# Kernel optimization log

Measured on AMD Instinct MI355X. Metric: run time of the kernel, lower is better.

The kernel has to match this reference:

```python
import jax, jax.numpy as jnp
import numpy as np
from functools import partial

EPS = 1e-8

@partial(jax.custom_vjp, nondiff_argnums=(2, 3))
def ste_quantize(x, scale, clamp_min, clamp_max):
    # forward: clamp(round(x/scale), min, max); backward: grad/scale (STE)
    return jnp.clip(jnp.round(x / scale), clamp_min, clamp_max)

def _ste_fwd(x, scale, clamp_min, clamp_max):
    return ste_quantize(x, scale, clamp_min, clamp_max), scale

def _ste_bwd(clamp_min, clamp_max, scale, g):
    return (g / scale, jnp.zeros_like(scale))

ste_quantize.defvjp(_ste_fwd, _ste_bwd)


def setup_inputs() -> dict:
    key = jax.random.key(0)
    kx, kw = jax.random.split(key)
    x = jax.random.normal(kx, (4, 4096, 2048), dtype=jnp.float32)
    # nn.init.normal_(weight, mean=0.0, std=0.006)
    weight = 0.006 * jax.random.normal(kw, (2048, 2048), dtype=jnp.float32)
    return {"x": x, "weight": weight}


def reference(x, weight):
    # per-tensor ternary weight quantization: alpha = mean(|W|)
    alpha = jnp.maximum(jnp.mean(jnp.abs(weight)), EPS)
    w_q = ste_quantize(weight, alpha, -1.0, 1.0)  # (out, in), values in {-1,0,1}
    # per-token int8 activation quantization: beta = max(|x|)/127
    beta = jnp.maximum(jnp.max(jnp.abs(x), axis=-1, keepdims=True) / 127.0, EPS)  # (b,s,1)
    x_q = ste_quantize(x, beta, -127.0, 127.0)  # (b,s,in)
    # fp32 GEMM on quantized values, then dequant rescale
    y = jnp.einsum('bsi,oi->bso', x_q, w_q)
    return y * alpha * beta
```

## Files before the change

kernel.cpp:

```cpp
#include <hip/hip_runtime.h>

#define IN_DIM 2048
#define OUT_DIM 2048
#define EPS 1e-8f

#define BK 128
#define NKT (IN_DIM / BK)
#define HALF 16384

using int32x4 = __attribute__((ext_vector_type(4))) int;

__global__ __launch_bounds__(256) void absum_kernel(const float* __restrict__ w,
                                                    double* __restrict__ sum, int n4) {
    int tid = blockIdx.x * blockDim.x + threadIdx.x;
    int stride = gridDim.x * blockDim.x;
    float s = 0.f;
    for (int i = tid; i < n4; i += stride) {
        float4 v = ((const float4*)w)[i];
        s += fabsf(v.x) + fabsf(v.y) + fabsf(v.z) + fabsf(v.w);
    }
    for (int off = 32; off; off >>= 1) s += __shfl_down(s, off);
    __shared__ float wsum[4];
    int lane = threadIdx.x & 63, wave = threadIdx.x >> 6;
    if (lane == 0) wsum[wave] = s;
    __syncthreads();
    if (threadIdx.x == 0) {
        double t = (double)wsum[0] + (double)wsum[1] + (double)wsum[2] + (double)wsum[3];
        atomicAdd(sum, t);
    }
}

__global__ __launch_bounds__(256) void quantw_kernel(const float* __restrict__ w,
                                                     const double* __restrict__ sumptr,
                                                     signed char* __restrict__ wq,
                                                     float* __restrict__ alpha_out, int n4) {
    float alpha = fmaxf((float)(*sumptr * (1.0 / (double)(IN_DIM * OUT_DIM))), EPS);
    int i = blockIdx.x * blockDim.x + threadIdx.x;
    if (i == 0) *alpha_out = alpha;
    if (i >= n4) return;
    float4 v = ((const float4*)w)[i];
    char4 q;
    q.x = (signed char)fminf(fmaxf(rintf(v.x / alpha), -1.f), 1.f);
    q.y = (signed char)fminf(fmaxf(rintf(v.y / alpha), -1.f), 1.f);
    q.z = (signed char)fminf(fmaxf(rintf(v.z / alpha), -1.f), 1.f);
    q.w = (signed char)fminf(fmaxf(rintf(v.w / alpha), -1.f), 1.f);
    ((char4*)wq)[i] = q;
}

__global__ __launch_bounds__(256) void quantx_kernel(const float* __restrict__ x,
                                                     signed char* __restrict__ xq,
                                                     float* __restrict__ beta_arr,
                                                     int tokens) {
    const int lane = threadIdx.x & 63;
    const int wave = threadIdx.x >> 6;
    const int t = blockIdx.x * 4 + wave;
    if (t >= tokens) return;

    const float4* row = (const float4*)(x + (size_t)t * IN_DIM);
    float4 v[8];
    float m = 0.f;
#pragma unroll
    for (int j = 0; j < 8; ++j) {
        v[j] = row[lane + 64 * j];
        m = fmaxf(m, fmaxf(fmaxf(fabsf(v[j].x), fabsf(v[j].y)),
                           fmaxf(fabsf(v[j].z), fabsf(v[j].w))));
    }
#pragma unroll
    for (int off = 32; off; off >>= 1) m = fmaxf(m, __shfl_xor(m, off));
    const float beta = fmaxf(m * (1.f / 127.f), EPS);
    if (lane == 0) beta_arr[t] = beta;

    char4* orow = (char4*)(xq + (size_t)t * IN_DIM);
#pragma unroll
    for (int j = 0; j < 8; ++j) {
        char4 q;
        q.x = (signed char)fminf(fmaxf(rintf(v[j].x / beta), -127.f), 127.f);
        q.y = (signed char)fminf(fmaxf(rintf(v[j].y / beta), -127.f), 127.f);
        q.z = (signed char)fminf(fmaxf(rintf(v[j].z / beta), -127.f), 127.f);
        q.w = (signed char)fminf(fmaxf(rintf(v[j].w / beta), -127.f), 127.f);
        orow[lane + 64 * j] = q;
    }
}

__device__ __forceinline__ void gll(const signed char* g, signed char* l) {
    __builtin_amdgcn_global_load_lds((const __attribute__((address_space(1))) void*)g,
        (__attribute__((address_space(3))) void*)l, 16, 0, 0);
}

#define CLUSTER(BASE, AF)                                                                      \
    __builtin_amdgcn_s_setprio(1);                                                             \
    _Pragma("unroll")                                                                          \
    for (int m_ = 0; m_ < 4; ++m_)                                                             \
        _Pragma("unroll")                                                                      \
        for (int n_ = 0; n_ < 4; ++n_)                                                         \
            acc[(BASE) + m_][n_] = __builtin_amdgcn_mfma_i32_16x16x64_i8(                      \
                AF[m_], bf[n_], acc[(BASE) + m_][n_], 0, 0, 0);                                \
    __builtin_amdgcn_s_setprio(0);

template<bool STG, bool TAIL>
__device__ __forceinline__ void ktile(int T, signed char* lds, int32x4 (&acc)[8][4],
                                      int aoff, int boff, int f0, int f1,
                                      const signed char* a0, const signed char* a1,
                                      const signed char* b0, const signed char* b1) {
    const int s = (T & 1) * HALF;
    const int d = ((T + 1) & 1) * HALF;
    const size_t ko = (size_t)(T + 1) * BK;
    int32x4 af0[4], af1[4], bf[4];

#pragma unroll
    for (int m = 0; m < 4; ++m) af0[m] = *(const int32x4*)(lds + s + aoff + m * 1024);
#pragma unroll
    for (int n = 0; n < 4; ++n) bf[n] = *(const int32x4*)(lds + 65536 + s + boff + n * 1024);
    if constexpr (STG) { gll(a0 + ko, lds + d + f0); gll(a1 + ko, lds + d + f1); }
#pragma unroll
    for (int m = 0; m < 4; ++m) af1[m] = *(const int32x4*)(lds + s + aoff + 4096 + m * 1024);
    CLUSTER(0, af0)
    if constexpr (STG) { gll(b0 + ko, lds + 65536 + d + f0); gll(b1 + ko, lds + 65536 + d + f1); }
    CLUSTER(4, af1)
    if constexpr (TAIL) asm volatile("s_waitcnt vmcnt(0)" ::: "memory");
    else                asm volatile("s_waitcnt vmcnt(4)" ::: "memory");
    __builtin_amdgcn_s_barrier();

#pragma unroll
    for (int m = 0; m < 4; ++m) af0[m] = *(const int32x4*)(lds + 32768 + s + aoff + m * 1024);
#pragma unroll
    for (int n = 0; n < 4; ++n) bf[n] = *(const int32x4*)(lds + 98304 + s + boff + n * 1024);
    if constexpr (STG) { gll(a0 + ko + 64, lds + 32768 + d + f0); gll(a1 + ko + 64, lds + 32768 + d + f1); }
#pragma unroll
    for (int m = 0; m < 4; ++m) af1[m] = *(const int32x4*)(lds + 32768 + s + aoff + 4096 + m * 1024);
    CLUSTER(0, af0)
    if constexpr (STG) { gll(b0 + ko + 64, lds + 98304 + d + f0); gll(b1 + ko + 64, lds + 98304 + d + f1); }
    CLUSTER(4, af1)
    if constexpr (!TAIL) {
        asm volatile("s_waitcnt vmcnt(4)" ::: "memory");
        __builtin_amdgcn_s_barrier();
    }
}

__global__ __launch_bounds__(512, 2) void gemm_kernel(const signed char* __restrict__ xq,
                                                      const signed char* __restrict__ wq,
                                                      const float* __restrict__ beta,
                                                      const float* __restrict__ alpha_p,
                                                      float* __restrict__ out) {
    extern __shared__ signed char lds[];
    const int tid = threadIdx.x;
    const int lane = tid & 63;
    const int wave = tid >> 6;
    const int wm = wave >> 2;
    const int wn = wave & 3;
    const int row0 = blockIdx.x * 256;
    const int col0 = blockIdx.y * 256;

    const int f0 = tid * 16;
    const int f1 = f0 + 8192;
    const int g0 = f0 >> 10, kg0 = (f0 >> 8) & 3, r0 = (f0 >> 4) & 15;
    const int g1 = f1 >> 10, kg1 = (f1 >> 8) & 3, r1 = (f1 >> 4) & 15;
    const signed char* a0 = xq + (size_t)(row0 + g0 * 16 + r0) * IN_DIM + kg0 * 16;
    const signed char* a1 = xq + (size_t)(row0 + g1 * 16 + r1) * IN_DIM + kg1 * 16;
    const signed char* b0 = wq + (size_t)(col0 + g0 * 16 + r0) * IN_DIM + kg0 * 16;
    const signed char* b1 = wq + (size_t)(col0 + g1 * 16 + r1) * IN_DIM + kg1 * 16;

    const int kr = (lane >> 4) * 256 + (lane & 15) * 16;
    const int aoff = wm * 8192 + kr;
    const int boff = wn * 4096 + kr;

    int32x4 acc[8][4] = {};

    gll(a0, lds + f0);              gll(a1, lds + f1);
    gll(b0, lds + 65536 + f0);      gll(b1, lds + 65536 + f1);
    gll(a0 + 64, lds + 32768 + f0); gll(a1 + 64, lds + 32768 + f1);
    gll(b0 + 64, lds + 98304 + f0); gll(b1 + 64, lds + 98304 + f1);
    asm volatile("s_waitcnt vmcnt(4)" ::: "memory");
    __builtin_amdgcn_s_barrier();

    for (int T = 0; T < NKT - 1; ++T)
        ktile<true, false>(T, lds, acc, aoff, boff, f0, f1, a0, a1, b0, b1);
    ktile<false, true>(NKT - 1, lds, acc, aoff, boff, f0, f1, a0, a1, b0, b1);

    const float alpha = *alpha_p;
#pragma unroll
    for (int mi = 0; mi < 8; ++mi) {
        int rbase = row0 + wm * 128 + mi * 16 + ((lane >> 4) << 2);
#pragma unroll
        for (int r = 0; r < 4; ++r) {
            int row = rbase + r;
            float scale = alpha * beta[row];
#pragma unroll
            for (int n = 0; n < 4; ++n) {
                int col = col0 + wn * 64 + n * 16 + (lane & 15);
                out[(size_t)row * OUT_DIM + col] = (float)acc[mi][n][r] * scale;
            }
        }
    }
}

extern "C" void kernel_launch(void* const* d_in, const int* in_sizes, int n_in,
                              void* d_out, int out_size, void* d_ws, size_t ws_size,
                              hipStream_t stream) {
    const float* x = (const float*)d_in[0];
    const float* w = (const float*)d_in[1];
    float* out = (float*)d_out;

    const int tokens = in_sizes[0] / IN_DIM;
    const int n_w = in_sizes[1];
    const int n_w4 = n_w / 4;

    char* ws = (char*)d_ws;
    double* d_sum = (double*)ws;
    float* d_alpha = (float*)(ws + 8);
    float* d_beta = (float*)(ws + 256);
    signed char* d_wq = (signed char*)(ws + 256 + 65536);
    signed char* d_xq = d_wq + (size_t)n_w;

    hipMemsetAsync(d_ws, 0, 16, stream);

    absum_kernel<<<1024, 256, 0, stream>>>(w, d_sum, n_w4);
    quantw_kernel<<<(n_w4 + 255) / 256, 256, 0, stream>>>(w, d_sum, d_wq, d_alpha, n_w4);
    quantx_kernel<<<(tokens + 3) / 4, 256, 0, stream>>>(x, d_xq, d_beta, tokens);

    hipFuncSetAttribute((const void*)gemm_kernel,
                        hipFuncAttributeMaxDynamicSharedMemorySize, 131072);

    dim3 grid(16384 / 256, OUT_DIM / 256);
    gemm_kernel<<<grid, 512, 131072, stream>>>(d_xq, d_wq, d_beta, d_alpha, out);
}
```

Measured before the change: 149.5 us.

## Use 4 waves with 128x128 per-wave tiles in int8 GEMM

Result: no change. 147.8 us (-1.2%).

```diff
diff --git a/kernel.cpp b/kernel.cpp
--- a/kernel.cpp
+++ b/kernel.cpp
@@ -87,57 +87,76 @@
         (__attribute__((address_space(3))) void*)l, 16, 0, 0);
 }
 
-#define CLUSTER(BASE, AF)                                                                      \
+#define CLUSTER(MB, NB)                                                                        \
     __builtin_amdgcn_s_setprio(1);                                                             \
     _Pragma("unroll")                                                                          \
     for (int m_ = 0; m_ < 4; ++m_)                                                             \
         _Pragma("unroll")                                                                      \
         for (int n_ = 0; n_ < 4; ++n_)                                                         \
-            acc[(BASE) + m_][n_] = __builtin_amdgcn_mfma_i32_16x16x64_i8(                      \
-                AF[m_], bf[n_], acc[(BASE) + m_][n_], 0, 0, 0);                                \
+            acc[(MB) + m_][(NB) + n_] = __builtin_amdgcn_mfma_i32_16x16x64_i8(                 \
+                af[(MB) + m_], bf[(NB) + n_], acc[(MB) + m_][(NB) + n_], 0, 0, 0);             \
     __builtin_amdgcn_s_setprio(0);
 
 template<bool STG, bool TAIL>
-__device__ __forceinline__ void ktile(int T, signed char* lds, int32x4 (&acc)[8][4],
-                                      int aoff, int boff, int f0, int f1,
-                                      const signed char* a0, const signed char* a1,
-                                      const signed char* b0, const signed char* b1) {
+__device__ __forceinline__ void ktile(int T, signed char* lds, int32x4 (&acc)[8][8],
+                                      int aoff, int boff, int f,
+                                      const signed char* (&aP)[4], const signed char* (&bP)[4]) {
     const int s = (T & 1) * HALF;
     const int d = ((T + 1) & 1) * HALF;
     const size_t ko = (size_t)(T + 1) * BK;
-    int32x4 af0[4], af1[4], bf[4];
-
-#pragma unroll
-    for (int m = 0; m < 4; ++m) af0[m] = *(const int32x4*)(lds + s + aoff + m * 1024);
+    int32x4 af[8], bf[8];
+
+#pragma unroll
+    for (int m = 0; m < 4; ++m) af[m] = *(const int32x4*)(lds + s + aoff + m * 1024);
 #pragma unroll
     for (int n = 0; n < 4; ++n) bf[n] = *(const int32x4*)(lds + 65536 + s + boff + n * 1024);
-    if constexpr (STG) { gll(a0 + ko, lds + d + f0); gll(a1 + ko, lds + d + f1); }
-#pragma unroll
-    for (int m = 0; m < 4; ++m) af1[m] = *(const int32x4*)(lds + s + aoff + 4096 + m * 1024);
-    CLUSTER(0, af0)
-    if constexpr (STG) { gll(b0 + ko, lds + 65536 + d + f0); gll(b1 + ko, lds + 65536 + d + f1); }
-    CLUSTER(4, af1)
+    if constexpr (STG) {
+#pragma unroll
+        for (int c = 0; c < 4; ++c) gll(aP[c] + ko, lds + d + f + c * 4096);
+    }
+#pragma unroll
+    for (int m = 0; m < 4; ++m) af[4 + m] = *(const int32x4*)(lds + s + aoff + 4096 + m * 1024);
+#pragma unroll
+    for (int n = 0; n < 4; ++n) bf[4 + n] = *(const int32x4*)(lds + 65536 + s + boff + 4096 + n * 1024);
+    CLUSTER(0, 0)
+    if constexpr (STG) {
+#pragma unroll
+        for (int c = 0; c < 4; ++c) gll(bP[c] + ko, lds + 65536 + d + f + c * 4096);
+    }
+    CLUSTER(0, 4)
+    CLUSTER(4, 0)
+    CLUSTER(4, 4)
     if constexpr (TAIL) asm volatile("s_waitcnt vmcnt(0)" ::: "memory");
-    else                asm volatile("s_waitcnt vmcnt(4)" ::: "memory");
+    else                asm volatile("s_waitcnt vmcnt(8)" ::: "memory");
     __builtin_amdgcn_s_barrier();
 
 #pragma unroll
-    for (int m = 0; m < 4; ++m) af0[m] = *(const int32x4*)(lds + 32768 + s + aoff + m * 1024);
+    for (int m = 0; m < 4; ++m) af[m] = *(const int32x4*)(lds + 32768 + s + aoff + m * 1024);
 #pragma unroll
     for (int n = 0; n < 4; ++n) bf[n] = *(const int32x4*)(lds + 98304 + s + boff + n * 1024);
-    if constexpr (STG) { gll(a0 + ko + 64, lds + 32768 + d + f0); gll(a1 + ko + 64, lds + 32768 + d + f1); }
-#pragma unroll
-    for (int m = 0; m < 4; ++m) af1[m] = *(const int32x4*)(lds + 32768 + s + aoff + 4096 + m * 1024);
-    CLUSTER(0, af0)
-    if constexpr (STG) { gll(b0 + ko + 64, lds + 98304 + d + f0); gll(b1 + ko + 64, lds + 98304 + d + f1); }
-    CLUSTER(4, af1)
+    if constexpr (STG) {
+#pragma unroll
+        for (int c = 0; c < 4; ++c) gll(aP[c] + ko + 64, lds + 32768 + d + f + c * 4096);
+    }
+#pragma unroll
+    for (int m = 0; m < 4; ++m) af[4 + m] = *(const int32x4*)(lds + 32768 + s + aoff + 4096 + m * 1024);
+#pragma unroll
+    for (int n = 0; n < 4; ++n) bf[4 + n] = *(const int32x4*)(lds + 98304 + s + boff + 4096 + n * 1024);
+    CLUSTER(0, 0)
+    if constexpr (STG) {
+#pragma unroll
+        for (int c = 0; c < 4; ++c) gll(bP[c] + ko + 64, lds + 98304 + d + f + c * 4096);
+    }
+    CLUSTER(0, 4)
+    CLUSTER(4, 0)
+    CLUSTER(4, 4)
     if constexpr (!TAIL) {
-        asm volatile("s_waitcnt vmcnt(4)" ::: "memory");
+        asm volatile("s_waitcnt vmcnt(8)" ::: "memory");
         __builtin_amdgcn_s_barrier();
     }
 }
 
-__global__ __launch_bounds__(512, 2) void gemm_kernel(const signed char* __restrict__ xq,
+__global__ __launch_bounds__(256, 1) void gemm_kernel(const signed char* __restrict__ xq,
                                                       const signed char* __restrict__ wq,
                                                       const float* __restrict__ beta,
                                                       const float* __restrict__ alpha_p,
@@ -146,36 +165,42 @@
     const int tid = threadIdx.x;
     const int lane = tid & 63;
     const int wave = tid >> 6;
-    const int wm = wave >> 2;
-    const int wn = wave & 3;
+    const int wm = wave >> 1;
+    const int wn = wave & 1;
     const int row0 = blockIdx.x * 256;
     const int col0 = blockIdx.y * 256;
 
-    const int f0 = tid * 16;
-    const int f1 = f0 + 8192;
-    const int g0 = f0 >> 10, kg0 = (f0 >> 8) & 3, r0 = (f0 >> 4) & 15;
-    const int g1 = f1 >> 10, kg1 = (f1 >> 8) & 3, r1 = (f1 >> 4) & 15;
-    const signed char* a0 = xq + (size_t)(row0 + g0 * 16 + r0) * IN_DIM + kg0 * 16;
-    const signed char* a1 = xq + (size_t)(row0 + g1 * 16 + r1) * IN_DIM + kg1 * 16;
-    const signed char* b0 = wq + (size_t)(col0 + g0 * 16 + r0) * IN_DIM + kg0 * 16;
-    const signed char* b1 = wq + (size_t)(col0 + g1 * 16 + r1) * IN_DIM + kg1 * 16;
+    const int f = tid * 16;
+    const int rowb = ((tid >> 6) << 4) + (tid & 15);
+    const int skg = ((tid >> 4) & 3) << 4;
+    const signed char* aP[4];
+    const signed char* bP[4];
+#pragma unroll
+    for (int c = 0; c < 4; ++c) {
+        aP[c] = xq + (size_t)(row0 + rowb + 64 * c) * IN_DIM + skg;
+        bP[c] = wq + (size_t)(col0 + rowb + 64 * c) * IN_DIM + skg;
+    }
 
     const int kr = (lane >> 4) * 256 + (lane & 15) * 16;
     const int aoff = wm * 8192 + kr;
-    const int boff = wn * 4096 + kr;
-
-    int32x4 acc[8][4] = {};
-
-    gll(a0, lds + f0);              gll(a1, lds + f1);
-    gll(b0, lds + 65536 + f0);      gll(b1, lds + 65536 + f1);
-    gll(a0 + 64, lds + 32768 + f0); gll(a1 + 64, lds + 32768 + f1);
-    gll(b0 + 64, lds + 98304 + f0); gll(b1 + 64, lds + 98304 + f1);
-    asm volatile("s_waitcnt vmcnt(4)" ::: "memory");
+    const int boff = wn * 8192 + kr;
+
+    int32x4 acc[8][8] = {};
+
+#pragma unroll
+    for (int c = 0; c < 4; ++c) gll(aP[c], lds + f + c * 4096);
+#pragma unroll
+    for (int c = 0; c < 4; ++c) gll(bP[c], lds + 65536 + f + c * 4096);
+#pragma unroll
+    for (int c = 0; c < 4; ++c) gll(aP[c] + 64, lds + 32768 + f + c * 4096);
+#pragma unroll
+    for (int c = 0; c < 4; ++c) gll(bP[c] + 64, lds + 98304 + f + c * 4096);
+    asm volatile("s_waitcnt vmcnt(8)" ::: "memory");
     __builtin_amdgcn_s_barrier();
 
     for (int T = 0; T < NKT - 1; ++T)
-        ktile<true, false>(T, lds, acc, aoff, boff, f0, f1, a0, a1, b0, b1);
-    ktile<false, true>(NKT - 1, lds, acc, aoff, boff, f0, f1, a0, a1, b0, b1);
+        ktile<true, false>(T, lds, acc, aoff, boff, f, aP, bP);
+    ktile<false, true>(NKT - 1, lds, acc, aoff, boff, f, aP, bP);
 
     const float alpha = *alpha_p;
 #pragma unroll
@@ -186,8 +211,8 @@
             int row = rbase + r;
             float scale = alpha * beta[row];
 #pragma unroll
-            for (int n = 0; n < 4; ++n) {
-                int col = col0 + wn * 64 + n * 16 + (lane & 15);
+            for (int n = 0; n < 8; ++n) {
+                int col = col0 + wn * 128 + n * 16 + (lane & 15);
                 out[(size_t)row * OUT_DIM + col] = (float)acc[mi][n][r] * scale;
             }
         }
@@ -222,5 +247,5 @@
                         hipFuncAttributeMaxDynamicSharedMemorySize, 131072);
 
     dim3 grid(16384 / 256, OUT_DIM / 256);
-    gemm_kernel<<<grid, 512, 131072, stream>>>(d_xq, d_wq, d_beta, d_alpha, out);
-}
+    gemm_kernel<<<grid, 256, 131072, stream>>>(d_xq, d_wq, d_beta, d_alpha, out);
+}
```

## Load weight fragments directly to registers and fuse activation quant with weight abs-sum

Applied to the files above, without the earlier changes.

Result: slower. 179.4 us (+20.0%).

```diff
diff --git a/kernel.cpp b/kernel.cpp
--- a/kernel.cpp
+++ b/kernel.cpp
@@ -10,23 +10,57 @@
 
 using int32x4 = __attribute__((ext_vector_type(4))) int;
 
-__global__ __launch_bounds__(256) void absum_kernel(const float* __restrict__ w,
-                                                    double* __restrict__ sum, int n4) {
-    int tid = blockIdx.x * blockDim.x + threadIdx.x;
-    int stride = gridDim.x * blockDim.x;
-    float s = 0.f;
-    for (int i = tid; i < n4; i += stride) {
-        float4 v = ((const float4*)w)[i];
-        s += fabsf(v.x) + fabsf(v.y) + fabsf(v.z) + fabsf(v.w);
-    }
-    for (int off = 32; off; off >>= 1) s += __shfl_down(s, off);
-    __shared__ float wsum[4];
-    int lane = threadIdx.x & 63, wave = threadIdx.x >> 6;
-    if (lane == 0) wsum[wave] = s;
-    __syncthreads();
-    if (threadIdx.x == 0) {
-        double t = (double)wsum[0] + (double)wsum[1] + (double)wsum[2] + (double)wsum[3];
-        atomicAdd(sum, t);
+__global__ __launch_bounds__(256) void prep_kernel(const float* __restrict__ x,
+                                                   signed char* __restrict__ xq,
+                                                   float* __restrict__ beta_arr,
+                                                   int tokens,
+                                                   const float* __restrict__ w,
+                                                   double* __restrict__ sum, int n4) {
+    if (blockIdx.x < 4096) {
+        const int lane = threadIdx.x & 63;
+        const int wave = threadIdx.x >> 6;
+        const int t = blockIdx.x * 4 + wave;
+        if (t >= tokens) return;
+        const float4* row = (const float4*)(x + (size_t)t * IN_DIM);
+        float4 v[8];
+        float m = 0.f;
+#pragma unroll
+        for (int j = 0; j < 8; ++j) {
+            v[j] = row[lane + 64 * j];
+            m = fmaxf(m, fmaxf(fmaxf(fabsf(v[j].x), fabsf(v[j].y)),
+                               fmaxf(fabsf(v[j].z), fabsf(v[j].w))));
+        }
+#pragma unroll
+        for (int off = 32; off; off >>= 1) m = fmaxf(m, __shfl_xor(m, off));
+        const float beta = fmaxf(m * (1.f / 127.f), EPS);
+        if (lane == 0) beta_arr[t] = beta;
+        char4* orow = (char4*)(xq + (size_t)t * IN_DIM);
+#pragma unroll
+        for (int j = 0; j < 8; ++j) {
+            char4 q;
+            q.x = (signed char)fminf(fmaxf(rintf(v[j].x / beta), -127.f), 127.f);
+            q.y = (signed char)fminf(fmaxf(rintf(v[j].y / beta), -127.f), 127.f);
+            q.z = (signed char)fminf(fmaxf(rintf(v[j].z / beta), -127.f), 127.f);
+            q.w = (signed char)fminf(fmaxf(rintf(v[j].w / beta), -127.f), 127.f);
+            orow[lane + 64 * j] = q;
+        }
+    } else {
+        int tid = (blockIdx.x - 4096) * blockDim.x + threadIdx.x;
+        int stride = 1024 * blockDim.x;
+        float s = 0.f;
+        for (int i = tid; i < n4; i += stride) {
+            float4 vv = ((const float4*)w)[i];
+            s += fabsf(vv.x) + fabsf(vv.y) + fabsf(vv.z) + fabsf(vv.w);
+        }
+        for (int off = 32; off; off >>= 1) s += __shfl_down(s, off);
+        __shared__ float wsum[4];
+        int lane = threadIdx.x & 63, wave = threadIdx.x >> 6;
+        if (lane == 0) wsum[wave] = s;
+        __syncthreads();
+        if (threadIdx.x == 0) {
+            double tt = (double)wsum[0] + (double)wsum[1] + (double)wsum[2] + (double)wsum[3];
+            atomicAdd(sum, tt);
+        }
     }
 }
 
@@ -47,94 +81,56 @@
     ((char4*)wq)[i] = q;
 }
 
-__global__ __launch_bounds__(256) void quantx_kernel(const float* __restrict__ x,
-                                                     signed char* __restrict__ xq,
-                                                     float* __restrict__ beta_arr,
-                                                     int tokens) {
-    const int lane = threadIdx.x & 63;
-    const int wave = threadIdx.x >> 6;
-    const int t = blockIdx.x * 4 + wave;
-    if (t >= tokens) return;
-
-    const float4* row = (const float4*)(x + (size_t)t * IN_DIM);
-    float4 v[8];
-    float m = 0.f;
-#pragma unroll
-    for (int j = 0; j < 8; ++j) {
-        v[j] = row[lane + 64 * j];
-        m = fmaxf(m, fmaxf(fmaxf(fabsf(v[j].x), fabsf(v[j].y)),
-                           fmaxf(fabsf(v[j].z), fabsf(v[j].w))));
-    }
-#pragma unroll
-    for (int off = 32; off; off >>= 1) m = fmaxf(m, __shfl_xor(m, off));
-    const float beta = fmaxf(m * (1.f / 127.f), EPS);
-    if (lane == 0) beta_arr[t] = beta;
-
-    char4* orow = (char4*)(xq + (size_t)t * IN_DIM);
-#pragma unroll
-    for (int j = 0; j < 8; ++j) {
-        char4 q;
-        q.x = (signed char)fminf(fmaxf(rintf(v[j].x / beta), -127.f), 127.f);
-        q.y = (signed char)fminf(fmaxf(rintf(v[j].y / beta), -127.f), 127.f);
-        q.z = (signed char)fminf(fmaxf(rintf(v[j].z / beta), -127.f), 127.f);
-        q.w = (signed char)fminf(fmaxf(rintf(v[j].w / beta), -127.f), 127.f);
-        orow[lane + 64 * j] = q;
-    }
-}
-
 __device__ __forceinline__ void gll(const signed char* g, signed char* l) {
     __builtin_amdgcn_global_load_lds((const __attribute__((address_space(1))) void*)g,
         (__attribute__((address_space(3))) void*)l, 16, 0, 0);
 }
 
-#define CLUSTER(BASE, AF)                                                                      \
+#define MFMA32(B)                                                                              \
     __builtin_amdgcn_s_setprio(1);                                                             \
     _Pragma("unroll")                                                                          \
-    for (int m_ = 0; m_ < 4; ++m_)                                                             \
+    for (int m_ = 0; m_ < 8; ++m_)                                                             \
         _Pragma("unroll")                                                                      \
         for (int n_ = 0; n_ < 4; ++n_)                                                         \
-            acc[(BASE) + m_][n_] = __builtin_amdgcn_mfma_i32_16x16x64_i8(                      \
-                AF[m_], bf[n_], acc[(BASE) + m_][n_], 0, 0, 0);                                \
+            acc[m_][n_] = __builtin_amdgcn_mfma_i32_16x16x64_i8(                               \
+                af[m_], B[n_], acc[m_][n_], 0, 0, 0);                                          \
     __builtin_amdgcn_s_setprio(0);
 
 template<bool STG, bool TAIL>
 __device__ __forceinline__ void ktile(int T, signed char* lds, int32x4 (&acc)[8][4],
-                                      int aoff, int boff, int f0, int f1,
-                                      const signed char* a0, const signed char* a1,
-                                      const signed char* b0, const signed char* b1) {
+                                      int32x4 (&bA)[4], int32x4 (&bB)[4],
+                                      const signed char* const (&bAddr)[4],
+                                      int aoff, int f0, int f1,
+                                      const signed char* a0, const signed char* a1) {
     const int s = (T & 1) * HALF;
     const int d = ((T + 1) & 1) * HALF;
-    const size_t ko = (size_t)(T + 1) * BK;
-    int32x4 af0[4], af1[4], bf[4];
-
-#pragma unroll
-    for (int m = 0; m < 4; ++m) af0[m] = *(const int32x4*)(lds + s + aoff + m * 1024);
-#pragma unroll
-    for (int n = 0; n < 4; ++n) bf[n] = *(const int32x4*)(lds + 65536 + s + boff + n * 1024);
-    if constexpr (STG) { gll(a0 + ko, lds + d + f0); gll(a1 + ko, lds + d + f1); }
-#pragma unroll
-    for (int m = 0; m < 4; ++m) af1[m] = *(const int32x4*)(lds + s + aoff + 4096 + m * 1024);
-    CLUSTER(0, af0)
-    if constexpr (STG) { gll(b0 + ko, lds + 65536 + d + f0); gll(b1 + ko, lds + 65536 + d + f1); }
-    CLUSTER(4, af1)
-    if constexpr (TAIL) asm volatile("s_waitcnt vmcnt(0)" ::: "memory");
-    else                asm volatile("s_waitcnt vmcnt(4)" ::: "memory");
+    const int ko = T * BK;
+    const int kn = (T + 1) * BK;
+    int32x4 af[8];
+
+#pragma unroll
+    for (int m = 0; m < 8; ++m) af[m] = *(const int32x4*)(lds + s + aoff + m * 1024);
+#pragma unroll
+    for (int n = 0; n < 4; ++n) bB[n] = *(const int32x4*)(bAddr[n] + ko + 64);
+    if constexpr (STG) { gll(a0 + kn, lds + d + f0); gll(a1 + kn, lds + d + f1); }
+    if constexpr (TAIL) asm volatile("s_waitcnt vmcnt(4)" ::: "memory");
+    else                asm volatile("s_waitcnt vmcnt(6)" ::: "memory");
+    MFMA32(bA)
     __builtin_amdgcn_s_barrier();
 
 #pragma unroll
-    for (int m = 0; m < 4; ++m) af0[m] = *(const int32x4*)(lds + 32768 + s + aoff + m * 1024);
-#pragma unroll
-    for (int n = 0; n < 4; ++n) bf[n] = *(const int32x4*)(lds + 98304 + s + boff + n * 1024);
-    if constexpr (STG) { gll(a0 + ko + 64, lds + 32768 + d + f0); gll(a1 + ko + 64, lds + 32768 + d + f1); }
-#pragma unroll
-    for (int m = 0; m < 4; ++m) af1[m] = *(const int32x4*)(lds + 32768 + s + aoff + 4096 + m * 1024);
-    CLUSTER(0, af0)
-    if constexpr (STG) { gll(b0 + ko + 64, lds + 98304 + d + f0); gll(b1 + ko + 64, lds + 98304 + d + f1); }
-    CLUSTER(4, af1)
+    for (int m = 0; m < 8; ++m) af[m] = *(const int32x4*)(lds + 32768 + s + aoff + m * 1024);
     if constexpr (!TAIL) {
-        asm volatile("s_waitcnt vmcnt(4)" ::: "memory");
-        __builtin_amdgcn_s_barrier();
+#pragma unroll
+        for (int n = 0; n < 4; ++n) bA[n] = *(const int32x4*)(bAddr[n] + kn);
+        if constexpr (STG) { gll(a0 + kn + 64, lds + 32768 + d + f0);
+                             gll(a1 + kn + 64, lds + 32768 + d + f1); }
+        asm volatile("s_waitcnt vmcnt(6)" ::: "memory");
+    } else {
+        asm volatile("s_waitcnt vmcnt(0)" ::: "memory");
     }
+    MFMA32(bB)
+    if constexpr (!TAIL) __builtin_amdgcn_s_barrier();
 }
 
 __global__ __launch_bounds__(512, 2) void gemm_kernel(const signed char* __restrict__ xq,
@@ -157,25 +153,29 @@
     const int g1 = f1 >> 10, kg1 = (f1 >> 8) & 3, r1 = (f1 >> 4) & 15;
     const signed char* a0 = xq + (size_t)(row0 + g0 * 16 + r0) * IN_DIM + kg0 * 16;
     const signed char* a1 = xq + (size_t)(row0 + g1 * 16 + r1) * IN_DIM + kg1 * 16;
-    const signed char* b0 = wq + (size_t)(col0 + g0 * 16 + r0) * IN_DIM + kg0 * 16;
-    const signed char* b1 = wq + (size_t)(col0 + g1 * 16 + r1) * IN_DIM + kg1 * 16;
+
+    const signed char* bAddr[4];
+#pragma unroll
+    for (int n = 0; n < 4; ++n)
+        bAddr[n] = wq + (size_t)(col0 + wn * 64 + n * 16 + (lane & 15)) * IN_DIM
+                      + ((lane >> 4) << 4);
 
     const int kr = (lane >> 4) * 256 + (lane & 15) * 16;
     const int aoff = wm * 8192 + kr;
-    const int boff = wn * 4096 + kr;
 
     int32x4 acc[8][4] = {};
-
-    gll(a0, lds + f0);              gll(a1, lds + f1);
-    gll(b0, lds + 65536 + f0);      gll(b1, lds + 65536 + f1);
+    int32x4 bA[4], bB[4];
+
+    gll(a0, lds + f0);           gll(a1, lds + f1);
     gll(a0 + 64, lds + 32768 + f0); gll(a1 + 64, lds + 32768 + f1);
-    gll(b0 + 64, lds + 98304 + f0); gll(b1 + 64, lds + 98304 + f1);
-    asm volatile("s_waitcnt vmcnt(4)" ::: "memory");
+#pragma unroll
+    for (int n = 0; n < 4; ++n) bA[n] = *(const int32x4*)(bAddr[n]);
+    asm volatile("s_waitcnt vmcnt(0)" ::: "memory");
     __builtin_amdgcn_s_barrier();
 
     for (int T = 0; T < NKT - 1; ++T)
-        ktile<true, false>(T, lds, acc, aoff, boff, f0, f1, a0, a1, b0, b1);
-    ktile<false, true>(NKT - 1, lds, acc, aoff, boff, f0, f1, a0, a1, b0, b1);
+        ktile<true, false>(T, lds, acc, bA, bB, bAddr, aoff, f0, f1, a0, a1);
+    ktile<false, true>(NKT - 1, lds, acc, bA, bB, bAddr, aoff, f0, f1, a0, a1);
 
     const float alpha = *alpha_p;
 #pragma unroll
@@ -214,13 +214,12 @@
 
     hipMemsetAsync(d_ws, 0, 16, stream);
 
-    absum_kernel<<<1024, 256, 0, stream>>>(w, d_sum, n_w4);
+    prep_kernel<<<5120, 256, 0, stream>>>(x, d_xq, d_beta, tokens, w, d_sum, n_w4);
     quantw_kernel<<<(n_w4 + 255) / 256, 256, 0, stream>>>(w, d_sum, d_wq, d_alpha, n_w4);
-    quantx_kernel<<<(tokens + 3) / 4, 256, 0, stream>>>(x, d_xq, d_beta, tokens);
 
     hipFuncSetAttribute((const void*)gemm_kernel,
-                        hipFuncAttributeMaxDynamicSharedMemorySize, 131072);
+                        hipFuncAttributeMaxDynamicSharedMemorySize, 65536);
 
     dim3 grid(16384 / 256, OUT_DIM / 256);
-    gemm_kernel<<<grid, 512, 131072, stream>>>(d_xq, d_wq, d_beta, d_alpha, out);
-}
+    gemm_kernel<<<grid, 512, 65536, stream>>>(d_xq, d_wq, d_beta, d_alpha, out);
+}
```
